# Optimization experiments

Hardware: AMD Instinct MI355X
Metric: run time of the kernel (lower is better)

Reference implementation:

```python
import jax, jax.numpy as jnp
import numpy as np

V, E, H, L = 32000, 512, 1024, 2
B, T_DEC, S_ENC = 32, 64, 128
NEG = -1000000.0


def setup_inputs() -> dict:
    key = jax.random.key(0)
    ks = jax.random.split(key, 20)
    s = 0.02
    return {
        "X": jax.random.randint(ks[0], (B, T_DEC), 0, V),
        "enc_outputs": jax.random.normal(ks[1], (B, S_ENC, H), jnp.float32),
        "hidden_state": jax.random.normal(ks[2], (L, B, H), jnp.float32),
        "valid_lens": jax.random.randint(ks[3], (B,), 1, S_ENC),
        "emb": jax.random.normal(ks[4], (V, E), jnp.float32) * s,
        "Wq": jax.random.normal(ks[5], (H, H), jnp.float32) * s,
        "Wk": jax.random.normal(ks[6], (H, H), jnp.float32) * s,
        "wv": jax.random.normal(ks[7], (H,), jnp.float32) * s,
        "W_ih0": jax.random.normal(ks[8], (3 * H, H + E), jnp.float32) * s,
        "W_hh0": jax.random.normal(ks[9], (3 * H, H), jnp.float32) * s,
        "b_ih0": jnp.zeros((3 * H,), jnp.float32),
        "b_hh0": jnp.zeros((3 * H,), jnp.float32),
        "W_ih1": jax.random.normal(ks[10], (3 * H, H), jnp.float32) * s,
        "W_hh1": jax.random.normal(ks[11], (3 * H, H), jnp.float32) * s,
        "b_ih1": jnp.zeros((3 * H,), jnp.float32),
        "b_hh1": jnp.zeros((3 * H,), jnp.float32),
        "W_out": jax.random.normal(ks[12], (V, H), jnp.float32) * s,
        "b_out": jnp.zeros((V,), jnp.float32),
    }


def gru_cell(x, h, W_ih, W_hh, b_ih, b_hh):
    # PyTorch GRU cell gate math
    gi = x @ W_ih.T + b_ih
    gh = h @ W_hh.T + b_hh
    i_r, i_z, i_n = jnp.split(gi, 3, axis=-1)
    h_r, h_z, h_n = jnp.split(gh, 3, axis=-1)
    r = jax.nn.sigmoid(i_r + h_r)
    z = jax.nn.sigmoid(i_z + h_z)
    n = jnp.tanh(i_n + r * h_n)
    return (1.0 - z) * n + z * h


def reference(X, enc_outputs, hidden_state, valid_lens, emb, Wq, Wk, wv,
              W_ih0, W_hh0, b_ih0, b_hh0, W_ih1, W_hh1, b_ih1, b_hh1,
              W_out, b_out):
    # Precompute key projections once (same math as per-step recompute)
    keys_proj = enc_outputs @ Wk.T                       # [B,S,H]
    mask = jnp.arange(S_ENC)[None, :] < valid_lens[:, None]  # [B,S]
    xs = emb[X].transpose(1, 0, 2)                       # [T,B,E]

    def step(h, x_t):
        q = h[-1] @ Wq.T                                 # [B,H] query = top-layer hidden
        scores = jnp.einsum('bsh,h->bs', jnp.tanh(q[:, None, :] + keys_proj), wv)
        scores = jnp.where(mask, scores, NEG)
        attn = jax.nn.softmax(scores, axis=-1)           # [B,S]
        ctx = jnp.einsum('bs,bsh->bh', attn, enc_outputs)
        inp = jnp.concatenate([ctx, x_t], axis=-1)       # [B,H+E]
        h0 = gru_cell(inp, h[0], W_ih0, W_hh0, b_ih0, b_hh0)
        h1 = gru_cell(h0, h[1], W_ih1, W_hh1, b_ih1, b_hh1)
        return jnp.stack([h0, h1]), h1

    _, outs = jax.lax.scan(step, hidden_state, xs)       # outs: [T,B,H]
    logits = outs @ W_out.T + b_out                      # [T,B,V]
    return logits.transpose(1, 0, 2)                     # [B,T,V]
```

## Files before the change

### kernel.cpp

```cpp
#include <hip/hip_runtime.h>


#define BB 32
#define TT 64
#define SS 128
#define HH 1024
#define EE 512
#define VV 32000
#define H3 3072
#define NEGV (-1000000.0f)
#define NB 1024

typedef __attribute__((ext_vector_type(8))) unsigned short u16x8;
typedef __attribute__((ext_vector_type(4))) unsigned short u16x4;
typedef __attribute__((ext_vector_type(8))) short s16x8;
typedef __attribute__((ext_vector_type(4))) float f32x4;

__device__ __forceinline__ unsigned short f2bf(float f) {
  unsigned int u = __builtin_bit_cast(unsigned int, f);
  unsigned int r = (u + 0x7FFFu + ((u >> 16) & 1u)) >> 16;
  return (unsigned short)r;
}
__device__ __forceinline__ float bfu(unsigned short u) {
  return __builtin_bit_cast(float, (unsigned int)u << 16);
}
__device__ __forceinline__ float sigm(float x) {
  return 1.f / (1.f + __expf(-x));
}
__device__ __forceinline__ float tanhfast(float x) {
  float ax = fabsf(x);
  float e = __expf(2.f * ax);
  float th = 1.f - 2.f / (e + 1.f);
  return copysignf(th, x);
}

#if defined(__has_builtin)
#if __has_builtin(__builtin_amdgcn_fdot2_f32_bf16)
#define HAVE_DOT2BF 1
#endif
#endif
#ifdef HAVE_DOT2BF
typedef __attribute__((ext_vector_type(2))) __bf16 bf16x2;
__device__ __forceinline__ float dot2bf(unsigned w, unsigned x, float c) {
  return __builtin_amdgcn_fdot2_f32_bf16(__builtin_bit_cast(bf16x2, w),
                                         __builtin_bit_cast(bf16x2, x), c,
                                         false);
}
#else
__device__ __forceinline__ float dot2bf(unsigned w, unsigned x, float c) {
  c = fmaf(bfu((unsigned short)(w & 0xffffu)),
           bfu((unsigned short)(x & 0xffffu)), c);
  c = fmaf(bfu((unsigned short)(w >> 16)), bfu((unsigned short)(x >> 16)), c);
  return c;
}
#endif
__device__ __forceinline__ void dot8(float& acc, uint4 w, uint4 x) {
  acc = dot2bf(w.x, x.x, acc); acc = dot2bf(w.y, x.y, acc);
  acc = dot2bf(w.z, x.z, acc); acc = dot2bf(w.w, x.w, acc);
}

__device__ __forceinline__ float ldu(const float* p) {
  return __hip_atomic_load((float*)p, __ATOMIC_RELAXED, __HIP_MEMORY_SCOPE_AGENT);
}
__device__ __forceinline__ void stu(float* p, float v) {
  __hip_atomic_store(p, v, __ATOMIC_RELAXED, __HIP_MEMORY_SCOPE_AGENT);
}
__device__ __forceinline__ unsigned long long ldu64(const unsigned short* p) {
  return __hip_atomic_load((const unsigned long long*)p, __ATOMIC_RELAXED,
                           __HIP_MEMORY_SCOPE_AGENT);
}
__device__ __forceinline__ void stu16(unsigned short* p, unsigned short v) {
  __hip_atomic_store(p, v, __ATOMIC_RELAXED, __HIP_MEMORY_SCOPE_AGENT);
}

__global__ __launch_bounds__(256) void k_init(const float* __restrict__ hid,
                                              unsigned short* __restrict__ h0A,
                                              unsigned short* __restrict__ h1i,
                                              unsigned* __restrict__ bar) {
  int i = blockIdx.x * 256 + threadIdx.x;
  if (i < BB * HH) h0A[i] = f2bf(hid[i]);
  else if (i < 2 * BB * HH) h1i[i - BB * HH] = f2bf(hid[i]);
  else if (i < 2 * BB * HH + 16896) bar[i - 2 * BB * HH] = 0u;
}

__global__ __launch_bounds__(256) void k_gather(const int* __restrict__ X,
                                                const float* __restrict__ emb,
                                                unsigned short* __restrict__ xs) {
  int idx = blockIdx.x * 256 + threadIdx.x;
  int r = idx >> 7, c4 = (idx & 127) << 2;
  int td = r >> 5, b = r & 31;
  int tok = X[b * TT + td];
  float4 v = *(const float4*)(emb + (size_t)tok * EE + c4);
  ushort4 o;
  o.x = f2bf(v.x); o.y = f2bf(v.y); o.z = f2bf(v.z); o.w = f2bf(v.w);
  *(ushort4*)(xs + (size_t)r * EE + c4) = o;
}

__global__ __launch_bounds__(256) void k_conv(const float* __restrict__ src,
                                              unsigned short* __restrict__ dst,
                                              int cols4, int ld) {
  int r = blockIdx.x;
  for (int c = threadIdx.x; c < cols4; c += 256) {
    float4 v = *(const float4*)(src + (size_t)r * ld + (size_t)c * 4);
    ushort4 o;
    o.x = f2bf(v.x); o.y = f2bf(v.y); o.z = f2bf(v.z); o.w = f2bf(v.w);
    *(ushort4*)(dst + (size_t)r * cols4 * 4 + (size_t)c * 4) = o;
  }
}

__global__ __launch_bounds__(256) void k_gemm_mfma(
    const unsigned short* __restrict__ A, const unsigned short* __restrict__ W,
    const float* __restrict__ bias, float* __restrict__ C,
    int M, int N, int K, int permuteBT, int outBF16) {
  __shared__ unsigned short As[128 * 32];
  __shared__ unsigned short Bs[128 * 32];
  const int m0 = blockIdx.y * 128, n0 = blockIdx.x * 128;
  const int t = threadIdx.x;
  const int lane = t & 63, w = t >> 6;
  const int wr = w >> 1, wc = w & 1;
  const int fr = lane & 15, fq = lane >> 4;
  const int srow = t >> 2;
  const int scol = (t & 3) * 8;
  f32x4 acc[4][4] = {};
  for (int k0 = 0; k0 < K; k0 += 32) {
#pragma unroll
    for (int i = 0; i < 2; ++i) {
      __builtin_amdgcn_global_load_lds(
          (const __attribute__((address_space(1))) void*)(A + (size_t)(m0 + i * 64 + srow) * K + k0 + scol),
          (__attribute__((address_space(3))) void*)((char*)As + i * 4096 + w * 1024),
          16, 0, 0);
      __builtin_amdgcn_global_load_lds(
          (const __attribute__((address_space(1))) void*)(W + (size_t)(n0 + i * 64 + srow) * K + k0 + scol),
          (__attribute__((address_space(3))) void*)((char*)Bs + i * 4096 + w * 1024),
          16, 0, 0);
    }
    __syncthreads();
    s16x8 af[4], bf[4];
#pragma unroll
    for (int mi = 0; mi < 4; ++mi)
      af[mi] = *(const s16x8*)(As + (wr * 64 + mi * 16 + fr) * 32 + fq * 8);
#pragma unroll
    for (int ni = 0; ni < 4; ++ni)
      bf[ni] = *(const s16x8*)(Bs + (wc * 64 + ni * 16 + fr) * 32 + fq * 8);
#pragma unroll
    for (int mi = 0; mi < 4; ++mi)
#pragma unroll
      for (int ni = 0; ni < 4; ++ni)
        acc[mi][ni] = __builtin_amdgcn_mfma_f32_16x16x32_bf16(
            af[mi], bf[ni], acc[mi][ni], 0, 0, 0);
    __syncthreads();
  }
#pragma unroll
  for (int mi = 0; mi < 4; ++mi) {
#pragma unroll
    for (int ni = 0; ni < 4; ++ni) {
      int gc = n0 + wc * 64 + ni * 16 + fr;
      float bv = bias ? bias[gc] : 0.f;
#pragma unroll
      for (int j = 0; j < 4; ++j) {
        int gm = m0 + wr * 64 + mi * 16 + fq * 4 + j;
        size_t ro = permuteBT ? ((size_t)((gm & 31) * TT + (gm >> 5))) * N
                              : (size_t)gm * N;
        float v = acc[mi][ni][j] + bv;
        if (outBF16) ((unsigned short*)C)[ro + gc] = f2bf(v);
        else         C[ro + gc] = v;
      }
    }
  }
}

__device__ __forceinline__ void gru_phase(
    int sl, int t, unsigned* sxu, const unsigned* syu,
    const unsigned short* __restrict__ xg,
    const unsigned short* __restrict__ wi, const unsigned short* __restrict__ wh,
    const unsigned short* __restrict__ gixrow, const float* __restrict__ bih,
    const float* __restrict__ bhh, unsigned short* __restrict__ hdst) {
  {
    unsigned long long vx = ldu64(xg + t * 4);
    sxu[t * 2] = (unsigned)vx; sxu[t * 2 + 1] = (unsigned)(vx >> 32);
  }
  __syncthreads();
  const int nl = t >> 3, q8 = t & 7;
  const int n = sl * 32 + nl;
  const unsigned short* wr = wi + (size_t)n * HH + q8 * 8;
  const unsigned short* hr = wh + (size_t)n * HH + q8 * 8;
  float air = 0, aiz = 0, ain = 0, ahr = 0, ahz = 0, ahn = 0;
#pragma unroll 2
  for (int j = 0; j < 16; ++j) {
    const int ku = q8 * 4 + j * 32;
    uint4 xv = *(const uint4*)(sxu + ku);
    uint4 yv = *(const uint4*)(syu + ku);
    const unsigned short* wj = wr + j * 64;
    const unsigned short* hj = hr + j * 64;
    dot8(air, *(const uint4*)(wj),           xv);
    dot8(aiz, *(const uint4*)(wj + 1048576), xv);
    dot8(ain, *(const uint4*)(wj + 2097152), xv);
    dot8(ahr, *(const uint4*)(hj),           yv);
    dot8(ahz, *(const uint4*)(hj + 1048576), yv);
    dot8(ahn, *(const uint4*)(hj + 2097152), yv);
  }
  air += __shfl_xor(air, 1); air += __shfl_xor(air, 2); air += __shfl_xor(air, 4);
  aiz += __shfl_xor(aiz, 1); aiz += __shfl_xor(aiz, 2); aiz += __shfl_xor(aiz, 4);
  ain += __shfl_xor(ain, 1); ain += __shfl_xor(ain, 2); ain += __shfl_xor(ain, 4);
  ahr += __shfl_xor(ahr, 1); ahr += __shfl_xor(ahr, 2); ahr += __shfl_xor(ahr, 4);
  ahz += __shfl_xor(ahz, 1); ahz += __shfl_xor(ahz, 2); ahz += __shfl_xor(ahz, 4);
  ahn += __shfl_xor(ahn, 1); ahn += __shfl_xor(ahn, 2); ahn += __shfl_xor(ahn, 4);
  if (q8 == 0) {
    float gr = air, gz = aiz, gn = ain;
    if (gixrow) {
      gr += bfu(__builtin_nontemporal_load(gixrow + n));
      gz += bfu(__builtin_nontemporal_load(gixrow + HH + n));
      gn += bfu(__builtin_nontemporal_load(gixrow + 2 * HH + n));
    }
    if (bih) { gr += bih[n]; gz += bih[HH + n]; gn += bih[2 * HH + n]; }
    float h_r = ahr + bhh[n], h_z = ahz + bhh[HH + n], h_n = ahn + bhh[2 * HH + n];
    float r = sigm(gr + h_r);
    float z = sigm(gz + h_z);
    float nn = tanhfast(gn + r * h_n);
    unsigned yw = syu[n >> 1];
    float hp = bfu((unsigned short)((n & 1) ? (yw >> 16) : (yw & 0xffffu)));
    stu16(hdst + n, f2bf((1.f - z) * nn + z * hp));
  }
}

__global__ __launch_bounds__(256, 4) void k_persist(
    const unsigned short* __restrict__ keysb,
    const unsigned short* __restrict__ encb,
    const unsigned short* __restrict__ gi0xb,
    const unsigned short* __restrict__ wqb,
    const unsigned short* __restrict__ wi0, const unsigned short* __restrict__ wh0,
    const unsigned short* __restrict__ wi1, const unsigned short* __restrict__ wh1,
    const float* __restrict__ wv, const int* __restrict__ vlen,
    const unsigned short* __restrict__ h1i,
    const float* __restrict__ bhh0, const float* __restrict__ bih1,
    const float* __restrict__ bhh1,
    float* __restrict__ partial, float* __restrict__ scores,
    unsigned short* __restrict__ ctxb,
    unsigned short* __restrict__ h0A, unsigned short* __restrict__ h0B,
    unsigned short* __restrict__ outsb,
    unsigned* __restrict__ bar) {
  __shared__ unsigned sh1u[512];
  __shared__ unsigned sh0u[512];
  __shared__ unsigned sxu[512];
  __shared__ float qs[32];
  __shared__ float aux[640];
  __shared__ unsigned short keysl[128 * 32];
  __shared__ unsigned short encl[128 * 32];
  const int bid = blockIdx.x, t = threadIdx.x;
  const int b = bid >> 5, sl = bid & 31;
  const int vb = vlen[b];
  unsigned* rel = bar + 16384;
  unsigned ep = 0;

  for (int i = t; i < 1024; i += 256) {
    int s = i >> 3, q = i & 3;
    if (i & 4) {
      *(u16x4*)(encl + s * 32 + q * 8) =
          *(const u16x4*)(encb + (size_t)(b * SS + s) * HH + sl * 32 + q * 8);
      *(u16x4*)(encl + s * 32 + q * 8 + 4) =
          *(const u16x4*)(encb + (size_t)(b * SS + s) * HH + sl * 32 + q * 8 + 4);
    } else {
      *(u16x4*)(keysl + s * 32 + q * 8) =
          *(const u16x4*)(keysb + (size_t)(b * SS + s) * HH + sl * 32 + q * 8);
      *(u16x4*)(keysl + s * 32 + q * 8 + 4) =
          *(const u16x4*)(keysb + (size_t)(b * SS + s) * HH + sl * 32 + q * 8 + 4);
    }
  }
  __syncthreads();

#define GBAR() do { ++ep; __syncthreads();                                     \
    if (t == 0)                                                                \
      __hip_atomic_store(bar + bid * 16, ep, __ATOMIC_RELAXED,                 \
                         __HIP_MEMORY_SCOPE_AGENT);                            \
    if (sl == 0) {                                                             \
      if (t < 32)                                                              \
        while (__hip_atomic_load(bar + (b * 32 + t) * 16, __ATOMIC_RELAXED,    \
                                 __HIP_MEMORY_SCOPE_AGENT) < ep)               \
          __builtin_amdgcn_s_sleep(1);                                         \
      __syncthreads();                                                         \
      if (t == 0)                                                              \
        __hip_atomic_store(rel + b * 16, ep, __ATOMIC_RELAXED,                 \
                           __HIP_MEMORY_SCOPE_AGENT);                          \
    } else if (t == 0) {                                                       \
      while (__hip_atomic_load(rel + b * 16, __ATOMIC_RELAXED,                 \
                               __HIP_MEMORY_SCOPE_AGENT) < ep)                 \
        __builtin_amdgcn_s_sleep(1);                                           \
    }                                                                          \
    __syncthreads(); } while (0)

  for (int td = 0; td < TT; ++td) {
    const unsigned short* h1old =
        td ? outsb + (size_t)(td - 1) * BB * HH : h1i;
    const unsigned short* h0old = (td & 1) ? h0B : h0A;
    unsigned short*       h0new = (td & 1) ? h0A : h0B;

    {
      {
        unsigned long long v1 = ldu64(h1old + b * HH + t * 4);
        unsigned long long v0 = ldu64(h0old + b * HH + t * 4);
        sh1u[t * 2] = (unsigned)v1; sh1u[t * 2 + 1] = (unsigned)(v1 >> 32);
        sh0u[t * 2] = (unsigned)v0; sh0u[t * 2 + 1] = (unsigned)(v0 >> 32);
      }
      __syncthreads();
      {
        const int nl = t >> 3, q8 = t & 7;
        const unsigned short* wr = wqb + (size_t)(sl * 32 + nl) * HH + q8 * 8;
        float acc = 0;
#pragma unroll 4
        for (int j = 0; j < 16; ++j) {
          const int ku = q8 * 4 + j * 32;
          uint4 xv = *(const uint4*)(sh1u + ku);
          dot8(acc, *(const uint4*)(wr + j * 64), xv);
        }
        acc += __shfl_xor(acc, 1); acc += __shfl_xor(acc, 2);
        acc += __shfl_xor(acc, 4);
        if (q8 == 0) qs[nl] = acc;
      }
      __syncthreads();
      const int s = t >> 1, hf = t & 1;
      if (s < vb) {
        const unsigned short* kr = keysl + s * 32 + hf * 16;
        const float* wvp = wv + sl * 32 + hf * 16;
        const float* qp = qs + hf * 16;
        float a = 0;
#pragma unroll
        for (int j = 0; j < 4; ++j) {
          u16x4 kv = *(const u16x4*)(kr + j * 4);
          float4 wvv = *(const float4*)(wvp + j * 4);
          a = fmaf(tanhfast(qp[j * 4 + 0] + bfu(kv[0])), wvv.x, a);
          a = fmaf(tanhfast(qp[j * 4 + 1] + bfu(kv[1])), wvv.y, a);
          a = fmaf(tanhfast(qp[j * 4 + 2] + bfu(kv[2])), wvv.z, a);
          a = fmaf(tanhfast(qp[j * 4 + 3] + bfu(kv[3])), wvv.w, a);
        }
        a += __shfl_xor(a, 1);
        if (hf == 0) stu(partial + ((size_t)(b * SS + s)) * 32 + sl, a);
      }
    }
    GBAR();

    if (t < 128) {
      const int s = sl * 4 + (t >> 5), g = t & 31;
      float a = 0;
      if (s < vb) {
        a = ldu(partial + ((size_t)(b * SS + s)) * 32 + g);
        a += __shfl_xor(a, 1); a += __shfl_xor(a, 2); a += __shfl_xor(a, 4);
        a += __shfl_xor(a, 8); a += __shfl_xor(a, 16);
      }
      if (g == 0) stu(scores + b * SS + s, (s < vb) ? a : NEGV);
    }
    GBAR();

    {
      if (t < SS) aux[t] = ldu(scores + b * SS + t);
      __syncthreads();
      float mx = aux[0];
      for (int s = 1; s < vb; ++s) mx = fmaxf(mx, aux[s]);
      float p = (t < SS) ? __expf(aux[t] - mx) : 0.f;
      __syncthreads();
      if (t < SS) aux[t] = p;
      __syncthreads();
      float sum = 0;
      for (int s = 0; s < vb; ++s) sum += aux[s];
      const float inv = 1.f / sum;
      const int cp = t & 15, sg = t >> 4;
      float a0 = 0, a1 = 0;
      const int send = min((sg + 1) * 8, vb);
      for (int s = sg * 8; s < send; ++s) {
        unsigned e2 = *(const unsigned*)(encl + s * 32 + cp * 2);
        float pp = aux[s];
        a0 = fmaf(pp, bfu((unsigned short)(e2 & 0xffffu)), a0);
        a1 = fmaf(pp, bfu((unsigned short)(e2 >> 16)), a1);
      }
      aux[SS + sg * 32 + cp * 2]     = a0;
      aux[SS + sg * 32 + cp * 2 + 1] = a1;
      __syncthreads();
      if (t < 32) {
        float v = 0;
#pragma unroll
        for (int g2 = 0; g2 < 16; ++g2) v += aux[SS + g2 * 32 + t];
        stu16(ctxb + b * HH + sl * 32 + t, f2bf(v * inv));
      }
    }
    GBAR();

    gru_phase(sl, t, sxu, sh0u, ctxb + b * HH, wi0, wh0,
              gi0xb + ((size_t)td * BB + b) * H3, nullptr, bhh0,
              h0new + b * HH);
    GBAR();

    gru_phase(sl, t, sxu, sh1u, h0new + b * HH, wi1, wh1,
              nullptr, bih1, bhh1, outsb + (size_t)td * BB * HH + b * HH);
    GBAR();
  }
#undef GBAR
}

extern "C" void kernel_launch(void* const* d_in, const int* in_sizes, int n_in,
                              void* d_out, int out_size, void* d_ws,
                              size_t ws_size, hipStream_t stream) {
  const int*   X    = (const int*)  d_in[0];
  const float* enc  = (const float*)d_in[1];
  const float* hid  = (const float*)d_in[2];
  const int*   vlen = (const int*)  d_in[3];
  const float* emb  = (const float*)d_in[4];
  const float* Wq   = (const float*)d_in[5];
  const float* Wk   = (const float*)d_in[6];
  const float* wv   = (const float*)d_in[7];
  const float* Wih0 = (const float*)d_in[8];
  const float* Whh0 = (const float*)d_in[9];
  const float* bih0 = (const float*)d_in[10];
  const float* bhh0 = (const float*)d_in[11];
  const float* Wih1 = (const float*)d_in[12];
  const float* Whh1 = (const float*)d_in[13];
  const float* bih1 = (const float*)d_in[14];
  const float* bhh1 = (const float*)d_in[15];
  const float* Wout = (const float*)d_in[16];
  const float* bout = (const float*)d_in[17];
  float* out = (float*)d_out;

  float* ws = (float*)d_ws;
  unsigned short* wi0b   = (unsigned short*)ws;
  unsigned short* wh0b   = wi0b + (size_t)3145728;
  unsigned short* wi1b   = wh0b + (size_t)3145728;
  unsigned short* wh1b   = wi1b + (size_t)3145728;
  unsigned short* wqb    = (unsigned short*)(ws + 6291456);
  unsigned short* gi0xb  = (unsigned short*)(ws + 6815744);
  unsigned short* keysb  = (unsigned short*)(ws + 9961472);
  unsigned short* encb   = (unsigned short*)(ws + 12058624);
  unsigned short* xsb    = (unsigned short*)(ws + 14155776);
  unsigned short* wkb    = (unsigned short*)(ws + 14680064);
  unsigned short* wih0xb = (unsigned short*)(ws + 15204352);
  unsigned short* woutb  = (unsigned short*)ws;
  unsigned short* outsb  = (unsigned short*)(ws + 16384000);
  unsigned short* h0A    = (unsigned short*)(ws + 17432576);
  unsigned short* h0B    = (unsigned short*)(ws + 17448960);
  unsigned short* h1i    = (unsigned short*)(ws + 17465344);
  unsigned short* ctxb   = (unsigned short*)(ws + 17481728);
  float*          partial= ws + 17498112;
  float*          scores = ws + 17629184;
  unsigned*       bar    = (unsigned*)(ws + 17633280);

  k_init<<<322, 256, 0, stream>>>(hid, h0A, h1i, bar);
  k_gather<<<1024, 256, 0, stream>>>(X, emb, xsb);
  k_conv<<<4096, 256, 0, stream>>>(enc, encb, 256, HH);
  k_conv<<<1024, 256, 0, stream>>>(Wk, wkb, 256, HH);
  k_conv<<<3072, 256, 0, stream>>>(Wih0 + HH, wih0xb, 128, HH + EE);
  k_gemm_mfma<<<dim3(8, 32), 256, 0, stream>>>(encb, wkb, nullptr,
                                               (float*)keysb, BB * SS, HH, HH,
                                               0, 1);
  k_gemm_mfma<<<dim3(24, 16), 256, 0, stream>>>(xsb, wih0xb, bih0,
                                                (float*)gi0xb, TT * BB, H3, EE,
                                                0, 1);
  k_conv<<<1024, 256, 0, stream>>>(Wq, wqb, 256, HH);
  k_conv<<<3072, 256, 0, stream>>>(Wih0, wi0b, 256, HH + EE);
  k_conv<<<3072, 256, 0, stream>>>(Whh0, wh0b, 256, HH);
  k_conv<<<3072, 256, 0, stream>>>(Wih1, wi1b, 256, HH);
  k_conv<<<3072, 256, 0, stream>>>(Whh1, wh1b, 256, HH);

  k_persist<<<NB, 256, 0, stream>>>(keysb, encb, gi0xb, wqb,
                                    wi0b, wh0b, wi1b, wh1b,
                                    wv, vlen, h1i,
                                    bhh0, bih1, bhh1,
                                    partial, scores, ctxb, h0A, h0B, outsb, bar);

  k_conv<<<32000, 256, 0, stream>>>(Wout, woutb, 256, HH);
  k_gemm_mfma<<<dim3(250, 16), 256, 0, stream>>>(outsb, woutb, bout, out,
                                                 TT * BB, VV, HH, 1, 0);
}
```

Before: 4.420 ms.

## Pack four batch rows per persistent block to cut grid barrier participants

The persistent recurrent kernel now launches 256 blocks of 1024 threads. Each block handles four batch rows for the same hidden slice, where before there were 1024 blocks of 256 threads with one row each. Grid barriers now coordinate 8 groups of 32 blocks instead of 32 groups, and each weight slice loaded per block serves four batch rows from cache. The per-block LDS staging of keys and encoder slices is dropped, so attention reads them from global memory each step. That adds memory traffic and lowers occupancy per CU.

```diff
diff --git a/kernel.cpp b/kernel.cpp
--- a/kernel.cpp
+++ b/kernel.cpp
@@ -9,7 +9,8 @@
 #define VV 32000
 #define H3 3072
 #define NEGV (-1000000.0f)
-#define NB 1024
+#define NB 256
+#define NT 1024
 
 typedef __attribute__((ext_vector_type(8))) unsigned short u16x8;
 typedef __attribute__((ext_vector_type(4))) unsigned short u16x4;
@@ -80,7 +81,7 @@
   int i = blockIdx.x * 256 + threadIdx.x;
   if (i < BB * HH) h0A[i] = f2bf(hid[i]);
   else if (i < 2 * BB * HH) h1i[i - BB * HH] = f2bf(hid[i]);
-  else if (i < 2 * BB * HH + 16896) bar[i - 2 * BB * HH] = 0u;
+  else if (i < 2 * BB * HH + 4224) bar[i - 2 * BB * HH] = 0u;
 }
 
 __global__ __launch_bounds__(256) void k_gather(const int* __restrict__ X,
@@ -170,17 +171,17 @@
 }
 
 __device__ __forceinline__ void gru_phase(
-    int sl, int t, unsigned* sxu, const unsigned* syu,
+    int sl, int lb, int tl, unsigned* sxu, const unsigned* syu,
     const unsigned short* __restrict__ xg,
     const unsigned short* __restrict__ wi, const unsigned short* __restrict__ wh,
     const unsigned short* __restrict__ gixrow, const float* __restrict__ bih,
     const float* __restrict__ bhh, unsigned short* __restrict__ hdst) {
   {
-    unsigned long long vx = ldu64(xg + t * 4);
-    sxu[t * 2] = (unsigned)vx; sxu[t * 2 + 1] = (unsigned)(vx >> 32);
+    unsigned long long vx = ldu64(xg + tl * 4);
+    sxu[tl * 2] = (unsigned)vx; sxu[tl * 2 + 1] = (unsigned)(vx >> 32);
   }
   __syncthreads();
-  const int nl = t >> 3, q8 = t & 7;
+  const int nl = tl >> 3, q8 = tl & 7;
   const int n = sl * 32 + nl;
   const unsigned short* wr = wi + (size_t)n * HH + q8 * 8;
   const unsigned short* hr = wh + (size_t)n * HH + q8 * 8;
@@ -223,7 +224,7 @@
   }
 }
 
-__global__ __launch_bounds__(256, 4) void k_persist(
+__global__ __launch_bounds__(1024, 1) void k_persist(
     const unsigned short* __restrict__ keysb,
     const unsigned short* __restrict__ encb,
     const unsigned short* __restrict__ gi0xb,
@@ -239,34 +240,18 @@
     unsigned short* __restrict__ h0A, unsigned short* __restrict__ h0B,
     unsigned short* __restrict__ outsb,
     unsigned* __restrict__ bar) {
-  __shared__ unsigned sh1u[512];
-  __shared__ unsigned sh0u[512];
-  __shared__ unsigned sxu[512];
-  __shared__ float qs[32];
-  __shared__ float aux[640];
-  __shared__ unsigned short keysl[128 * 32];
-  __shared__ unsigned short encl[128 * 32];
+  __shared__ unsigned sh1u[4][512];
+  __shared__ unsigned sh0u[4][512];
+  __shared__ unsigned sxu[4][512];
+  __shared__ float qs[4][32];
+  __shared__ float aux[4][640];
   const int bid = blockIdx.x, t = threadIdx.x;
-  const int b = bid >> 5, sl = bid & 31;
+  const int bg = bid >> 5, sl = bid & 31;
+  const int lb = t >> 8, tl = t & 255;
+  const int b = bg * 4 + lb;
   const int vb = vlen[b];
-  unsigned* rel = bar + 16384;
+  unsigned* rel = bar + 4096;
   unsigned ep = 0;
-
-  for (int i = t; i < 1024; i += 256) {
-    int s = i >> 3, q = i & 3;
-    if (i & 4) {
-      *(u16x4*)(encl + s * 32 + q * 8) =
-          *(const u16x4*)(encb + (size_t)(b * SS + s) * HH + sl * 32 + q * 8);
-      *(u16x4*)(encl + s * 32 + q * 8 + 4) =
-          *(const u16x4*)(encb + (size_t)(b * SS + s) * HH + sl * 32 + q * 8 + 4);
-    } else {
-      *(u16x4*)(keysl + s * 32 + q * 8) =
-          *(const u16x4*)(keysb + (size_t)(b * SS + s) * HH + sl * 32 + q * 8);
-      *(u16x4*)(keysl + s * 32 + q * 8 + 4) =
-          *(const u16x4*)(keysb + (size_t)(b * SS + s) * HH + sl * 32 + q * 8 + 4);
-    }
-  }
-  __syncthreads();
 
 #define GBAR() do { ++ep; __syncthreads();                                     \
     if (t == 0)                                                                \
@@ -274,15 +259,15 @@
                          __HIP_MEMORY_SCOPE_AGENT);                            \
     if (sl == 0) {                                                             \
       if (t < 32)                                                              \
-        while (__hip_atomic_load(bar + (b * 32 + t) * 16, __ATOMIC_RELAXED,    \
+        while (__hip_atomic_load(bar + (bg * 32 + t) * 16, __ATOMIC_RELAXED,   \
                                  __HIP_MEMORY_SCOPE_AGENT) < ep)               \
           __builtin_amdgcn_s_sleep(1);                                         \
       __syncthreads();                                                         \
       if (t == 0)                                                              \
-        __hip_atomic_store(rel + b * 16, ep, __ATOMIC_RELAXED,                 \
+        __hip_atomic_store(rel + bg * 16, ep, __ATOMIC_RELAXED,                \
                            __HIP_MEMORY_SCOPE_AGENT);                          \
     } else if (t == 0) {                                                       \
-      while (__hip_atomic_load(rel + b * 16, __ATOMIC_RELAXED,                 \
+      while (__hip_atomic_load(rel + bg * 16, __ATOMIC_RELAXED,                \
                                __HIP_MEMORY_SCOPE_AGENT) < ep)                 \
         __builtin_amdgcn_s_sleep(1);                                           \
     }                                                                          \
@@ -296,32 +281,35 @@
 
     {
       {
-        unsigned long long v1 = ldu64(h1old + b * HH + t * 4);
-        unsigned long long v0 = ldu64(h0old + b * HH + t * 4);
-        sh1u[t * 2] = (unsigned)v1; sh1u[t * 2 + 1] = (unsigned)(v1 >> 32);
-        sh0u[t * 2] = (unsigned)v0; sh0u[t * 2 + 1] = (unsigned)(v0 >> 32);
+        unsigned long long v1 = ldu64(h1old + (size_t)b * HH + tl * 4);
+        unsigned long long v0 = ldu64(h0old + (size_t)b * HH + tl * 4);
+        sh1u[lb][tl * 2] = (unsigned)v1;
+        sh1u[lb][tl * 2 + 1] = (unsigned)(v1 >> 32);
+        sh0u[lb][tl * 2] = (unsigned)v0;
+        sh0u[lb][tl * 2 + 1] = (unsigned)(v0 >> 32);
       }
       __syncthreads();
       {
-        const int nl = t >> 3, q8 = t & 7;
+        const int nl = tl >> 3, q8 = tl & 7;
         const unsigned short* wr = wqb + (size_t)(sl * 32 + nl) * HH + q8 * 8;
         float acc = 0;
 #pragma unroll 4
         for (int j = 0; j < 16; ++j) {
           const int ku = q8 * 4 + j * 32;
-          uint4 xv = *(const uint4*)(sh1u + ku);
+          uint4 xv = *(const uint4*)(&sh1u[lb][ku]);
           dot8(acc, *(const uint4*)(wr + j * 64), xv);
         }
         acc += __shfl_xor(acc, 1); acc += __shfl_xor(acc, 2);
         acc += __shfl_xor(acc, 4);
-        if (q8 == 0) qs[nl] = acc;
-      }
-      __syncthreads();
-      const int s = t >> 1, hf = t & 1;
+        if (q8 == 0) qs[lb][nl] = acc;
+      }
+      __syncthreads();
+      const int s = tl >> 1, hf = tl & 1;
       if (s < vb) {
-        const unsigned short* kr = keysl + s * 32 + hf * 16;
+        const unsigned short* kr =
+            keysb + (size_t)(b * SS + s) * HH + sl * 32 + hf * 16;
         const float* wvp = wv + sl * 32 + hf * 16;
-        const float* qp = qs + hf * 16;
+        const float* qp = &qs[lb][hf * 16];
         float a = 0;
 #pragma unroll
         for (int j = 0; j < 4; ++j) {
@@ -338,8 +326,8 @@
     }
     GBAR();
 
-    if (t < 128) {
-      const int s = sl * 4 + (t >> 5), g = t & 31;
+    if (tl < 128) {
+      const int s = sl * 4 + (tl >> 5), g = tl & 31;
       float a = 0;
       if (s < vb) {
         a = ldu(partial + ((size_t)(b * SS + s)) * 32 + g);
@@ -351,45 +339,48 @@
     GBAR();
 
     {
-      if (t < SS) aux[t] = ldu(scores + b * SS + t);
-      __syncthreads();
-      float mx = aux[0];
-      for (int s = 1; s < vb; ++s) mx = fmaxf(mx, aux[s]);
-      float p = (t < SS) ? __expf(aux[t] - mx) : 0.f;
-      __syncthreads();
-      if (t < SS) aux[t] = p;
+      if (tl < SS) aux[lb][tl] = ldu(scores + b * SS + tl);
+      __syncthreads();
+      float mx = aux[lb][0];
+      for (int s = 1; s < vb; ++s) mx = fmaxf(mx, aux[lb][s]);
+      float p = (tl < SS) ? __expf(aux[lb][tl] - mx) : 0.f;
+      __syncthreads();
+      if (tl < SS) aux[lb][tl] = p;
       __syncthreads();
       float sum = 0;
-      for (int s = 0; s < vb; ++s) sum += aux[s];
+      for (int s = 0; s < vb; ++s) sum += aux[lb][s];
       const float inv = 1.f / sum;
-      const int cp = t & 15, sg = t >> 4;
+      const int cp = tl & 15, sg = tl >> 4;
       float a0 = 0, a1 = 0;
       const int send = min((sg + 1) * 8, vb);
       for (int s = sg * 8; s < send; ++s) {
-        unsigned e2 = *(const unsigned*)(encl + s * 32 + cp * 2);
-        float pp = aux[s];
+        unsigned e2 = *(const unsigned*)(
+            encb + (size_t)(b * SS + s) * HH + sl * 32 + cp * 2);
+        float pp = aux[lb][s];
         a0 = fmaf(pp, bfu((unsigned short)(e2 & 0xffffu)), a0);
         a1 = fmaf(pp, bfu((unsigned short)(e2 >> 16)), a1);
       }
-      aux[SS + sg * 32 + cp * 2]     = a0;
-      aux[SS + sg * 32 + cp * 2 + 1] = a1;
-      __syncthreads();
-      if (t < 32) {
+      __syncthreads();
+      aux[lb][SS + sg * 32 + cp * 2]     = a0;
+      aux[lb][SS + sg * 32 + cp * 2 + 1] = a1;
+      __syncthreads();
+      if (tl < 32) {
         float v = 0;
 #pragma unroll
-        for (int g2 = 0; g2 < 16; ++g2) v += aux[SS + g2 * 32 + t];
-        stu16(ctxb + b * HH + sl * 32 + t, f2bf(v * inv));
+        for (int g2 = 0; g2 < 16; ++g2) v += aux[lb][SS + g2 * 32 + tl];
+        stu16(ctxb + (size_t)b * HH + sl * 32 + tl, f2bf(v * inv));
       }
     }
     GBAR();
 
-    gru_phase(sl, t, sxu, sh0u, ctxb + b * HH, wi0, wh0,
+    gru_phase(sl, lb, tl, sxu[lb], sh0u[lb], ctxb + (size_t)b * HH, wi0, wh0,
               gi0xb + ((size_t)td * BB + b) * H3, nullptr, bhh0,
-              h0new + b * HH);
+              h0new + (size_t)b * HH);
     GBAR();
 
-    gru_phase(sl, t, sxu, sh1u, h0new + b * HH, wi1, wh1,
-              nullptr, bih1, bhh1, outsb + (size_t)td * BB * HH + b * HH);
+    gru_phase(sl, lb, tl, sxu[lb], sh1u[lb], h0new + (size_t)b * HH, wi1, wh1,
+              nullptr, bih1, bhh1,
+              outsb + (size_t)td * BB * HH + (size_t)b * HH);
     GBAR();
   }
 #undef GBAR
@@ -440,7 +431,7 @@
   float*          scores = ws + 17629184;
   unsigned*       bar    = (unsigned*)(ws + 17633280);
 
-  k_init<<<322, 256, 0, stream>>>(hid, h0A, h1i, bar);
+  k_init<<<273, 256, 0, stream>>>(hid, h0A, h1i, bar);
   k_gather<<<1024, 256, 0, stream>>>(X, emb, xsb);
   k_conv<<<4096, 256, 0, stream>>>(enc, encb, 256, HH);
   k_conv<<<1024, 256, 0, stream>>>(Wk, wkb, 256, HH);
@@ -457,11 +448,11 @@
   k_conv<<<3072, 256, 0, stream>>>(Wih1, wi1b, 256, HH);
   k_conv<<<3072, 256, 0, stream>>>(Whh1, wh1b, 256, HH);
 
-  k_persist<<<NB, 256, 0, stream>>>(keysb, encb, gi0xb, wqb,
-                                    wi0b, wh0b, wi1b, wh1b,
-                                    wv, vlen, h1i,
-                                    bhh0, bih1, bhh1,
-                                    partial, scores, ctxb, h0A, h0B, outsb, bar);
+  k_persist<<<NB, NT, 0, stream>>>(keysb, encb, gi0xb, wqb,
+                                   wi0b, wh0b, wi1b, wh1b,
+                                   wv, vlen, h1i,
+                                   bhh0, bih1, bhh1,
+                                   partial, scores, ctxb, h0A, h0B, outsb, bar);
 
   k_conv<<<32000, 256, 0, stream>>>(Wout, woutb, 256, HH);
   k_gemm_mfma<<<dim3(250, 16), 256, 0, stream>>>(outsb, woutb, bout, out,
```

Measured after the change: 5.475 ms. +23.9%, slower.
